# Kernel tuning notes

Measured on AMD Instinct MI355X. Metric: run time of the kernel, lower is better.

## Reference

```python
import jax, jax.numpy as jnp
import numpy as np

E = 32        # num_local_experts
TOP_K = 4     # num_experts_per_tok
H = 1024      # hidden_size
I = 1024      # intermediate_size (expert_dim)
ALPHA = 1.702
LIMIT = 7.0
B, S = 2, 1024


def setup_inputs() -> dict:
    key = jax.random.key(0)
    ks = jax.random.split(key, 8)
    scale = 0.02
    return {
        "hidden_states": jax.random.normal(ks[0], (B, S, H), dtype=jnp.float32),
        "gate_up_proj": jax.random.normal(ks[1], (E, H, 2 * I), dtype=jnp.float32) * scale,
        "gate_up_proj_bias": jax.random.normal(ks[2], (E, 2 * I), dtype=jnp.float32) * scale,
        "down_proj": jax.random.normal(ks[3], (E, I, H), dtype=jnp.float32) * scale,
        "down_proj_bias": jax.random.normal(ks[4], (E, H), dtype=jnp.float32) * scale,
        "router_weight": jax.random.normal(ks[5], (E, H), dtype=jnp.float32) * scale,
        "router_bias": jax.random.normal(ks[6], (E,), dtype=jnp.float32) * scale,
    }


def reference(hidden_states, gate_up_proj, gate_up_proj_bias, down_proj,
              down_proj_bias, router_weight, router_bias):
    b, s, h = hidden_states.shape
    x = hidden_states.reshape(-1, h)                       # [T, H], T = B*S
    t = x.shape[0]

    # ---- router: linear -> topk -> softmax over topk -> scatter to dense scores
    router_logits = x @ router_weight.T + router_bias      # [T, E]
    top_vals, top_idx = jax.lax.top_k(router_logits, TOP_K)
    top_w = jax.nn.softmax(top_vals, axis=-1)
    router_scores = jnp.zeros_like(router_logits).at[
        jnp.arange(t)[:, None], top_idx].set(top_w)        # [T, E]

    # ---- experts (dense all-expert path, interleaved gate/up columns)
    gate_w = gate_up_proj[..., 0::2]                       # [E, H, I]
    up_w = gate_up_proj[..., 1::2]                         # [E, H, I]
    gate_b = gate_up_proj_bias[..., 0::2]                  # [E, I]
    up_b = gate_up_proj_bias[..., 1::2]                    # [E, I]

    gate = jnp.einsum('th,ehi->eti', x, gate_w) + gate_b[:, None, :]
    up = jnp.einsum('th,ehi->eti', x, up_w) + up_b[:, None, :]
    gate = jnp.minimum(gate, LIMIT)
    up = jnp.clip(up, -LIMIT, LIMIT)
    glu = gate * jax.nn.sigmoid(gate * ALPHA)
    next_states = jnp.einsum('eti,eih->eth', (up + 1.0) * glu, down_proj)
    next_states = next_states + down_proj_bias[:, None, :]  # [E, T, H]

    # ---- combine: weight each expert output by its routing score and sum
    routed = jnp.einsum('eth,te->th', next_states, router_scores)
    return routed.reshape(b, s, h), router_scores
```

## Files before the change

kernel.cpp:

```cpp
#include <hip/hip_runtime.h>
#include <cstdint>
#include <cstddef>

#define E_ 32
#define TOPK_ 4
#define H_ 1024
#define I_ 1024
#define T_ 2048
#define ALPHA_ 1.702f
#define LIMIT_ 7.0f
#define BK_ 32
#define BKP_ 40

typedef __attribute__((ext_vector_type(8))) short s8;
typedef __attribute__((ext_vector_type(4))) float f4;

__device__ __forceinline__ unsigned short f2bf(float f) {
  unsigned int u = __float_as_uint(f);
  return (unsigned short)((u + 0x7fffu + ((u >> 16) & 1u)) >> 16);
}

__global__ __launch_bounds__(128)
void router_kernel(const float* __restrict__ x,
                   const float* __restrict__ rw,
                   const float* __restrict__ rb,
                   float* __restrict__ scores,
                   int* __restrict__ counts,
                   int* __restrict__ tok_list,
                   float* __restrict__ w_list) {
  int t = blockIdx.x;
  int tid = threadIdx.x;
  __shared__ float partial[128];
  __shared__ float logits[E_];
  int e = tid & 31, q = tid >> 5;
  const float* xp = x + (size_t)t * H_;
  const float* wp = rw + (size_t)e * H_ + q * 256;
  float s = 0.f;
  #pragma unroll 8
  for (int h = 0; h < 256; ++h) s += xp[q * 256 + h] * wp[h];
  partial[tid] = s;
  __syncthreads();
  if (tid < 32)
    logits[tid] = partial[tid] + partial[tid + 32] + partial[tid + 64] +
                  partial[tid + 96] + rb[tid];
  __syncthreads();
  if (tid == 0) {
    float l[E_];
    #pragma unroll
    for (int i = 0; i < E_; ++i) l[i] = logits[i];
    int idx[TOPK_]; float v[TOPK_];
    for (int k = 0; k < TOPK_; ++k) {
      int bi = 0; float bv = -1e30f;
      for (int i = 0; i < E_; ++i)
        if (l[i] > bv) { bv = l[i]; bi = i; }
      idx[k] = bi; v[k] = bv; l[bi] = -1e30f;
    }
    float m = v[0], den = 0.f, w[TOPK_];
    for (int k = 0; k < TOPK_; ++k) { w[k] = expf(v[k] - m); den += w[k]; }
    float inv = 1.f / den;
    float* srow = scores + (size_t)t * E_;
    #pragma unroll
    for (int i = 0; i < E_; ++i) srow[i] = 0.f;
    for (int k = 0; k < TOPK_; ++k) {
      float wk = w[k] * inv;
      srow[idx[k]] = wk;
      int pos = atomicAdd(&counts[idx[k]], 1);
      tok_list[idx[k] * T_ + pos] = t * TOPK_ + k;
      w_list[idx[k] * T_ + pos] = wk;
    }
  }
}

__global__ __launch_bounds__(256)
void gateup_mfma(const float* __restrict__ x,
                 const float* __restrict__ gw,
                 const float* __restrict__ gb,
                 const int* __restrict__ counts,
                 const int* __restrict__ tok_list,
                 unsigned short* __restrict__ act) {
  int e = blockIdx.z;
  int cnt = counts[e];
  int t0 = blockIdx.y * 64;
  if (t0 >= cnt) return;
  int itile = blockIdx.x;
  int tid = threadIdx.x;
  int lane = tid & 63;
  int wave = tid >> 6;
  int wm = wave >> 1, wn = wave & 1;

  __shared__ __align__(16) unsigned short Xs[2][64][BKP_];
  __shared__ __align__(16) unsigned short Wg[2][128][BKP_];
  __shared__ int toks[64];

  if (tid < 64) {
    int slot = t0 + tid;
    toks[tid] = (slot < cnt) ? tok_list[e * T_ + slot] : -1;
  }
  __syncthreads();

  f4 accg[2][2] = {};
  f4 accu[2][2] = {};

  int arow = tid >> 2;
  int akq  = (tid & 3) * 8;
  int aenc = toks[arow];
  const float* axp = (aenc >= 0) ? (x + (size_t)(aenc >> 2) * H_ + akq) : nullptr;
  const float* wbase = gw + (size_t)e * H_ * (2 * I_) + itile * 128;
  int n0 = tid & 127, koct0 = tid >> 7;
  int drow0 = (n0 >> 1) + (n0 & 1) * 64;
  const float* wp0 = wbase + (size_t)koct0 * 8 * (2 * I_) + n0;

  int fm = lane & 15, ko = (lane >> 4) * 8;

  float pA[8];
  float pB[2][8];

  {
    if (aenc >= 0) {
      float4 q0 = *(const float4*)(axp);
      float4 q1 = *(const float4*)(axp + 4);
      pA[0]=q0.x; pA[1]=q0.y; pA[2]=q0.z; pA[3]=q0.w;
      pA[4]=q1.x; pA[5]=q1.y; pA[6]=q1.z; pA[7]=q1.w;
    }
    #pragma unroll
    for (int r = 0; r < 2; ++r) {
      const float* wp = wp0 + (size_t)r * 16 * (2 * I_);
      #pragma unroll
      for (int j = 0; j < 8; ++j) pB[r][j] = wp[(size_t)j * (2 * I_)];
    }
  }

  int buf = 0;
  for (int c = 0; c < H_ / BK_; ++c) {
    {
      s8 av = {};
      if (aenc >= 0) {
        #pragma unroll
        for (int j = 0; j < 8; ++j) av[j] = (short)f2bf(pA[j]);
      }
      *(s8*)&Xs[buf][arow][akq] = av;
      #pragma unroll
      for (int r = 0; r < 2; ++r) {
        s8 bv;
        #pragma unroll
        for (int j = 0; j < 8; ++j) bv[j] = (short)f2bf(pB[r][j]);
        *(s8*)&Wg[buf][drow0][(koct0 + r * 2) * 8] = bv;
      }
    }
    __syncthreads();
    if (c + 1 < H_ / BK_) {
      int k0 = (c + 1) * BK_;
      if (aenc >= 0) {
        float4 q0 = *(const float4*)(axp + k0);
        float4 q1 = *(const float4*)(axp + k0 + 4);
        pA[0]=q0.x; pA[1]=q0.y; pA[2]=q0.z; pA[3]=q0.w;
        pA[4]=q1.x; pA[5]=q1.y; pA[6]=q1.z; pA[7]=q1.w;
      }
      #pragma unroll
      for (int r = 0; r < 2; ++r) {
        const float* wp = wp0 + (size_t)(k0 + r * 16) * (2 * I_);
        #pragma unroll
        for (int j = 0; j < 8; ++j) pB[r][j] = wp[(size_t)j * (2 * I_)];
      }
    }
    {
      s8 a0 = *(s8*)&Xs[buf][wm * 32 + fm][ko];
      s8 a1 = *(s8*)&Xs[buf][wm * 32 + 16 + fm][ko];
      #pragma unroll
      for (int g = 0; g < 2; ++g) {
        s8 bg = *(s8*)&Wg[buf][wn * 32 + g * 16 + fm][ko];
        s8 bu = *(s8*)&Wg[buf][64 + wn * 32 + g * 16 + fm][ko];
        accg[0][g] = __builtin_amdgcn_mfma_f32_16x16x32_bf16(a0, bg, accg[0][g], 0, 0, 0);
        accg[1][g] = __builtin_amdgcn_mfma_f32_16x16x32_bf16(a1, bg, accg[1][g], 0, 0, 0);
        accu[0][g] = __builtin_amdgcn_mfma_f32_16x16x32_bf16(a0, bu, accu[0][g], 0, 0, 0);
        accu[1][g] = __builtin_amdgcn_mfma_f32_16x16x32_bf16(a1, bu, accu[1][g], 0, 0, 0);
      }
    }
    buf ^= 1;
  }

  int rq = lane >> 4;
  #pragma unroll
  for (int g = 0; g < 2; ++g) {
    int i = itile * 64 + wn * 32 + g * 16 + (lane & 15);
    float bg_ = gb[e * 2 * I_ + 2 * i];
    float bu_ = gb[e * 2 * I_ + 2 * i + 1];
    #pragma unroll
    for (int f = 0; f < 2; ++f) {
      #pragma unroll
      for (int r = 0; r < 4; ++r) {
        int m = wm * 32 + f * 16 + rq * 4 + r;
        int enc = toks[m];
        if (enc < 0) continue;
        float gv = accg[f][g][r] + bg_;
        float uv = accu[f][g][r] + bu_;
        gv = fminf(gv, LIMIT_);
        uv = fminf(fmaxf(uv, -LIMIT_), LIMIT_);
        float glu = gv / (1.f + __expf(-ALPHA_ * gv));
        act[(size_t)enc * I_ + i] = f2bf((uv + 1.f) * glu);
      }
    }
  }
}

__global__ __launch_bounds__(256)
void down_mfma(const unsigned short* __restrict__ act,
               const float* __restrict__ dw,
               const float* __restrict__ db,
               const int* __restrict__ counts,
               const int* __restrict__ tok_list,
               const float* __restrict__ w_list,
               float* __restrict__ dsout) {
  int e = blockIdx.z;
  int cnt = counts[e];
  int t0 = blockIdx.y * 64;
  if (t0 >= cnt) return;
  int htile = blockIdx.x;
  int tid = threadIdx.x;
  int lane = tid & 63;
  int wave = tid >> 6;
  int wm = wave >> 1, wn = wave & 1;

  __shared__ __align__(16) unsigned short Xs[2][64][BKP_];
  __shared__ __align__(16) unsigned short Wd[2][128][BKP_];
  __shared__ int toks[64];
  __shared__ float tws[64];

  if (tid < 64) {
    int slot = t0 + tid;
    bool ok = slot < cnt;
    toks[tid] = ok ? tok_list[e * T_ + slot] : -1;
    tws[tid]  = ok ? w_list[e * T_ + slot] : 0.f;
  }
  __syncthreads();

  f4 acc[2][4] = {};

  int arow = tid >> 2;
  int akq  = (tid & 3) * 8;
  int aenc = toks[arow];
  const unsigned short* axp = (aenc >= 0) ? (act + (size_t)aenc * I_ + akq) : nullptr;
  const float* wbase = dw + (size_t)e * I_ * H_ + htile * 128;
  int n0 = tid & 127, koct0 = tid >> 7;
  const float* wp0 = wbase + (size_t)koct0 * 8 * H_ + n0;

  int fm = lane & 15, ko = (lane >> 4) * 8;

  s8 pA = {};
  float pB[2][8];

  {
    if (aenc >= 0) pA = *(const s8*)(axp);
    #pragma unroll
    for (int r = 0; r < 2; ++r) {
      const float* wp = wp0 + (size_t)r * 16 * H_;
      #pragma unroll
      for (int j = 0; j < 8; ++j) pB[r][j] = wp[(size_t)j * H_];
    }
  }

  int buf = 0;
  for (int c = 0; c < I_ / BK_; ++c) {
    *(s8*)&Xs[buf][arow][akq] = pA;
    #pragma unroll
    for (int r = 0; r < 2; ++r) {
      s8 bv;
      #pragma unroll
      for (int j = 0; j < 8; ++j) bv[j] = (short)f2bf(pB[r][j]);
      *(s8*)&Wd[buf][n0][(koct0 + r * 2) * 8] = bv;
    }
    __syncthreads();
    if (c + 1 < I_ / BK_) {
      int k0 = (c + 1) * BK_;
      if (aenc >= 0) pA = *(const s8*)(axp + k0);
      #pragma unroll
      for (int r = 0; r < 2; ++r) {
        const float* wp = wp0 + (size_t)(k0 + r * 16) * H_;
        #pragma unroll
        for (int j = 0; j < 8; ++j) pB[r][j] = wp[(size_t)j * H_];
      }
    }
    {
      s8 a0 = *(s8*)&Xs[buf][wm * 32 + fm][ko];
      s8 a1 = *(s8*)&Xs[buf][wm * 32 + 16 + fm][ko];
      #pragma unroll
      for (int g = 0; g < 4; ++g) {
        s8 b = *(s8*)&Wd[buf][wn * 64 + g * 16 + fm][ko];
        acc[0][g] = __builtin_amdgcn_mfma_f32_16x16x32_bf16(a0, b, acc[0][g], 0, 0, 0);
        acc[1][g] = __builtin_amdgcn_mfma_f32_16x16x32_bf16(a1, b, acc[1][g], 0, 0, 0);
      }
    }
    buf ^= 1;
  }

  int rq = lane >> 4;
  #pragma unroll
  for (int g = 0; g < 4; ++g) {
    int h = htile * 128 + wn * 64 + g * 16 + (lane & 15);
    float bias = db[e * H_ + h];
    #pragma unroll
    for (int f = 0; f < 2; ++f) {
      #pragma unroll
      for (int r = 0; r < 4; ++r) {
        int m = wm * 32 + f * 16 + rq * 4 + r;
        int enc = toks[m];
        if (enc < 0) continue;
        dsout[(size_t)enc * H_ + h] = (acc[f][g][r] + bias) * tws[m];
      }
    }
  }
}

__global__ __launch_bounds__(256)
void combine_kernel(const float* __restrict__ dsout,
                    float* __restrict__ routed) {
  int idx = blockIdx.x * 256 + threadIdx.x;
  int t = idx >> 8;
  int h = (idx & 255) * 4;
  const float* base = dsout + (size_t)t * 4 * H_ + h;
  float4 a = *(const float4*)(base);
  float4 b = *(const float4*)(base + H_);
  float4 c = *(const float4*)(base + 2 * H_);
  float4 d = *(const float4*)(base + 3 * H_);
  float4 o;
  o.x = a.x + b.x + c.x + d.x;
  o.y = a.y + b.y + c.y + d.y;
  o.z = a.z + b.z + c.z + d.z;
  o.w = a.w + b.w + c.w + d.w;
  *(float4*)(routed + (size_t)t * H_ + h) = o;
}

extern "C" void kernel_launch(void* const* d_in, const int* in_sizes, int n_in,
                              void* d_out, int out_size, void* d_ws, size_t ws_size,
                              hipStream_t stream) {
  (void)in_sizes; (void)n_in; (void)out_size; (void)ws_size;
  const float* x    = (const float*)d_in[0];
  const float* gup  = (const float*)d_in[1];
  const float* gupb = (const float*)d_in[2];
  const float* dwn  = (const float*)d_in[3];
  const float* dwnb = (const float*)d_in[4];
  const float* rw   = (const float*)d_in[5];
  const float* rb   = (const float*)d_in[6];

  float* routed = (float*)d_out;
  float* scores = (float*)d_out + (size_t)T_ * H_;

  char* ws = (char*)d_ws;
  int*   counts   = (int*)ws;
  int*   tok_list = (int*)(ws + 256);
  float* w_list   = (float*)(ws + 256 + (size_t)E_ * T_ * 4);
  unsigned short* act = (unsigned short*)(ws + 256 + 2 * (size_t)E_ * T_ * 4);
  float* dsout = (float*)(ws + 256 + 2 * (size_t)E_ * T_ * 4
                          + (size_t)T_ * TOPK_ * I_ * 2);

  hipMemsetAsync(counts, 0, E_ * sizeof(int), stream);

  router_kernel<<<T_, 128, 0, stream>>>(x, rw, rb, scores, counts, tok_list, w_list);
  gateup_mfma<<<dim3(16, 32, 32), 256, 0, stream>>>(x, gup, gupb, counts, tok_list, act);
  down_mfma<<<dim3(8, 32, 32), 256, 0, stream>>>(act, dwn, dwnb, counts, tok_list, w_list, dsout);
  combine_kernel<<<(T_ * H_ / 4) / 256, 256, 0, stream>>>(dsout, routed);
}
```

Baseline: 674.3 us.

## Pre-transpose and cast expert weights to bf16 before the MFMA GEMMs

Adds pre-pass kernels that cast activations to bf16 and transpose/cast the gate-up weights (de-interleaving gate and up) and the down weights into K-contiguous bf16 layouts. The GEMM kernels can then load 16-byte bf16 vectors directly into LDS instead of doing strided scalar fp32 loads and per-block conversion repeated across token tiles. The router dot product is also vectorized with float4 loads. The trade-off is an extra full read of the fp32 weights and a bf16 write every call, and the down-GEMM output buffer now reuses the gate-up weight scratch region.

```diff
diff --git a/kernel.cpp b/kernel.cpp
--- a/kernel.cpp
+++ b/kernel.cpp
@@ -11,6 +11,7 @@
 #define LIMIT_ 7.0f
 #define BK_ 32
 #define BKP_ 40
+#define TP_ 66
 
 typedef __attribute__((ext_vector_type(8))) short s8;
 typedef __attribute__((ext_vector_type(4))) float f4;
@@ -18,6 +19,60 @@
 __device__ __forceinline__ unsigned short f2bf(float f) {
   unsigned int u = __float_as_uint(f);
   return (unsigned short)((u + 0x7fffu + ((u >> 16) & 1u)) >> 16);
+}
+
+__global__ __launch_bounds__(256)
+void cast_x_kernel(const float* __restrict__ x, unsigned short* __restrict__ xb) {
+  size_t i = (size_t)(blockIdx.x * 256 + threadIdx.x) * 8;
+  float4 a = *(const float4*)(x + i);
+  float4 b = *(const float4*)(x + i + 4);
+  s8 v;
+  v[0] = (short)f2bf(a.x); v[1] = (short)f2bf(a.y);
+  v[2] = (short)f2bf(a.z); v[3] = (short)f2bf(a.w);
+  v[4] = (short)f2bf(b.x); v[5] = (short)f2bf(b.y);
+  v[6] = (short)f2bf(b.z); v[7] = (short)f2bf(b.w);
+  *(s8*)(xb + i) = v;
+}
+
+__global__ __launch_bounds__(256)
+void transpose_cast(const float* __restrict__ src, unsigned short* __restrict__ dst,
+                    int src_rows, int src_cols, int deint) {
+  int e = blockIdx.z;
+  int c0 = blockIdx.x * 64;
+  int r0 = blockIdx.y * 64;
+  int tid = threadIdx.x;
+  __shared__ unsigned short ldsT[64][TP_];
+
+  const float* sp = src + (size_t)e * src_rows * src_cols
+                        + (size_t)r0 * src_cols + c0;
+  int r = tid >> 2, cq = tid & 3;
+  const float* rowp = sp + (size_t)r * src_cols + cq * 4;
+  #pragma unroll
+  for (int j = 0; j < 4; ++j) {
+    float4 v = *(const float4*)(rowp + j * 16);
+    int c = cq * 4 + j * 16;
+    ldsT[c + 0][r] = f2bf(v.x);
+    ldsT[c + 1][r] = f2bf(v.y);
+    ldsT[c + 2][r] = f2bf(v.z);
+    ldsT[c + 3][r] = f2bf(v.w);
+  }
+  __syncthreads();
+
+  int co = tid >> 2, hq = tid & 3;
+  s8 v0 = *(s8*)&ldsT[co][hq * 16];
+  s8 v1 = *(s8*)&ldsT[co][hq * 16 + 8];
+  int C = c0 + co;
+  size_t out_off;
+  if (deint) {
+    out_off = (size_t)e * src_cols * src_rows
+            + (size_t)(C & 1) * (src_cols >> 1) * src_rows
+            + (size_t)(C >> 1) * src_rows + r0 + hq * 16;
+  } else {
+    out_off = (size_t)e * src_cols * src_rows
+            + (size_t)C * src_rows + r0 + hq * 16;
+  }
+  *(s8*)(dst + out_off) = v0;
+  *(s8*)(dst + out_off + 8) = v1;
 }
 
 __global__ __launch_bounds__(128)
@@ -33,11 +88,14 @@
   __shared__ float partial[128];
   __shared__ float logits[E_];
   int e = tid & 31, q = tid >> 5;
-  const float* xp = x + (size_t)t * H_;
-  const float* wp = rw + (size_t)e * H_ + q * 256;
+  const float4* xp = (const float4*)(x + (size_t)t * H_ + q * 256);
+  const float4* wp = (const float4*)(rw + (size_t)e * H_ + q * 256);
   float s = 0.f;
   #pragma unroll 8
-  for (int h = 0; h < 256; ++h) s += xp[q * 256 + h] * wp[h];
+  for (int h = 0; h < 64; ++h) {
+    float4 a = xp[h], b = wp[h];
+    s += a.x * b.x + a.y * b.y + a.z * b.z + a.w * b.w;
+  }
   partial[tid] = s;
   __syncthreads();
   if (tid < 32)
@@ -72,8 +130,8 @@
 }
 
 __global__ __launch_bounds__(256)
-void gateup_mfma(const float* __restrict__ x,
-                 const float* __restrict__ gw,
+void gateup_mfma(const unsigned short* __restrict__ xb,
+                 const unsigned short* __restrict__ wgu,
                  const float* __restrict__ gb,
                  const int* __restrict__ counts,
                  const int* __restrict__ tok_list,
@@ -101,67 +159,32 @@
   f4 accg[2][2] = {};
   f4 accu[2][2] = {};
 
-  int arow = tid >> 2;
-  int akq  = (tid & 3) * 8;
-  int aenc = toks[arow];
-  const float* axp = (aenc >= 0) ? (x + (size_t)(aenc >> 2) * H_ + akq) : nullptr;
-  const float* wbase = gw + (size_t)e * H_ * (2 * I_) + itile * 128;
-  int n0 = tid & 127, koct0 = tid >> 7;
-  int drow0 = (n0 >> 1) + (n0 & 1) * 64;
-  const float* wp0 = wbase + (size_t)koct0 * 8 * (2 * I_) + n0;
+  int row = tid >> 2, q = tid & 3;
+  int aenc = toks[row];
+  const unsigned short* axp = xb + (size_t)(aenc >> 2) * H_ + q * 8;
+  const unsigned short* bp0 = wgu + (size_t)e * 2 * I_ * H_
+                            + (size_t)(itile * 64 + row) * H_ + q * 8;
+  const unsigned short* bp1 = bp0 + (size_t)I_ * H_;
 
   int fm = lane & 15, ko = (lane >> 4) * 8;
 
-  float pA[8];
-  float pB[2][8];
-
-  {
-    if (aenc >= 0) {
-      float4 q0 = *(const float4*)(axp);
-      float4 q1 = *(const float4*)(axp + 4);
-      pA[0]=q0.x; pA[1]=q0.y; pA[2]=q0.z; pA[3]=q0.w;
-      pA[4]=q1.x; pA[5]=q1.y; pA[6]=q1.z; pA[7]=q1.w;
-    }
-    #pragma unroll
-    for (int r = 0; r < 2; ++r) {
-      const float* wp = wp0 + (size_t)r * 16 * (2 * I_);
-      #pragma unroll
-      for (int j = 0; j < 8; ++j) pB[r][j] = wp[(size_t)j * (2 * I_)];
-    }
-  }
+  s8 pA = {};
+  s8 pB0, pB1;
+  if (aenc >= 0) pA = *(const s8*)axp;
+  pB0 = *(const s8*)bp0;
+  pB1 = *(const s8*)bp1;
 
   int buf = 0;
   for (int c = 0; c < H_ / BK_; ++c) {
-    {
-      s8 av = {};
-      if (aenc >= 0) {
-        #pragma unroll
-        for (int j = 0; j < 8; ++j) av[j] = (short)f2bf(pA[j]);
-      }
-      *(s8*)&Xs[buf][arow][akq] = av;
-      #pragma unroll
-      for (int r = 0; r < 2; ++r) {
-        s8 bv;
-        #pragma unroll
-        for (int j = 0; j < 8; ++j) bv[j] = (short)f2bf(pB[r][j]);
-        *(s8*)&Wg[buf][drow0][(koct0 + r * 2) * 8] = bv;
-      }
-    }
+    *(s8*)&Xs[buf][row][q * 8] = pA;
+    *(s8*)&Wg[buf][row][q * 8] = pB0;
+    *(s8*)&Wg[buf][64 + row][q * 8] = pB1;
     __syncthreads();
     if (c + 1 < H_ / BK_) {
       int k0 = (c + 1) * BK_;
-      if (aenc >= 0) {
-        float4 q0 = *(const float4*)(axp + k0);
-        float4 q1 = *(const float4*)(axp + k0 + 4);
-        pA[0]=q0.x; pA[1]=q0.y; pA[2]=q0.z; pA[3]=q0.w;
-        pA[4]=q1.x; pA[5]=q1.y; pA[6]=q1.z; pA[7]=q1.w;
-      }
-      #pragma unroll
-      for (int r = 0; r < 2; ++r) {
-        const float* wp = wp0 + (size_t)(k0 + r * 16) * (2 * I_);
-        #pragma unroll
-        for (int j = 0; j < 8; ++j) pB[r][j] = wp[(size_t)j * (2 * I_)];
-      }
+      if (aenc >= 0) pA = *(const s8*)(axp + k0);
+      pB0 = *(const s8*)(bp0 + k0);
+      pB1 = *(const s8*)(bp1 + k0);
     }
     {
       s8 a0 = *(s8*)&Xs[buf][wm * 32 + fm][ko];
@@ -205,7 +228,7 @@
 
 __global__ __launch_bounds__(256)
 void down_mfma(const unsigned short* __restrict__ act,
-               const float* __restrict__ dw,
+               const unsigned short* __restrict__ wdt,
                const float* __restrict__ db,
                const int* __restrict__ counts,
                const int* __restrict__ tok_list,
@@ -236,49 +259,32 @@
 
   f4 acc[2][4] = {};
 
-  int arow = tid >> 2;
-  int akq  = (tid & 3) * 8;
-  int aenc = toks[arow];
-  const unsigned short* axp = (aenc >= 0) ? (act + (size_t)aenc * I_ + akq) : nullptr;
-  const float* wbase = dw + (size_t)e * I_ * H_ + htile * 128;
-  int n0 = tid & 127, koct0 = tid >> 7;
-  const float* wp0 = wbase + (size_t)koct0 * 8 * H_ + n0;
+  int row = tid >> 2, q = tid & 3;
+  int aenc = toks[row];
+  const unsigned short* axp = act + (size_t)aenc * I_ + q * 8;
+  const unsigned short* bp0 = wdt + (size_t)e * H_ * I_
+                            + (size_t)(htile * 128 + row) * I_ + q * 8;
+  const unsigned short* bp1 = bp0 + (size_t)64 * I_;
 
   int fm = lane & 15, ko = (lane >> 4) * 8;
 
   s8 pA = {};
-  float pB[2][8];
-
-  {
-    if (aenc >= 0) pA = *(const s8*)(axp);
-    #pragma unroll
-    for (int r = 0; r < 2; ++r) {
-      const float* wp = wp0 + (size_t)r * 16 * H_;
-      #pragma unroll
-      for (int j = 0; j < 8; ++j) pB[r][j] = wp[(size_t)j * H_];
-    }
-  }
+  s8 pB0, pB1;
+  if (aenc >= 0) pA = *(const s8*)axp;
+  pB0 = *(const s8*)bp0;
+  pB1 = *(const s8*)bp1;
 
   int buf = 0;
   for (int c = 0; c < I_ / BK_; ++c) {
-    *(s8*)&Xs[buf][arow][akq] = pA;
-    #pragma unroll
-    for (int r = 0; r < 2; ++r) {
-      s8 bv;
-      #pragma unroll
-      for (int j = 0; j < 8; ++j) bv[j] = (short)f2bf(pB[r][j]);
-      *(s8*)&Wd[buf][n0][(koct0 + r * 2) * 8] = bv;
-    }
+    *(s8*)&Xs[buf][row][q * 8] = pA;
+    *(s8*)&Wd[buf][row][q * 8] = pB0;
+    *(s8*)&Wd[buf][64 + row][q * 8] = pB1;
     __syncthreads();
     if (c + 1 < I_ / BK_) {
       int k0 = (c + 1) * BK_;
       if (aenc >= 0) pA = *(const s8*)(axp + k0);
-      #pragma unroll
-      for (int r = 0; r < 2; ++r) {
-        const float* wp = wp0 + (size_t)(k0 + r * 16) * H_;
-        #pragma unroll
-        for (int j = 0; j < 8; ++j) pB[r][j] = wp[(size_t)j * H_];
-      }
+      pB0 = *(const s8*)(bp0 + k0);
+      pB1 = *(const s8*)(bp1 + k0);
     }
     {
       s8 a0 = *(s8*)&Xs[buf][wm * 32 + fm][ko];
@@ -347,16 +353,26 @@
 
   char* ws = (char*)d_ws;
   int*   counts   = (int*)ws;
-  int*   tok_list = (int*)(ws + 256);
-  float* w_list   = (float*)(ws + 256 + (size_t)E_ * T_ * 4);
-  unsigned short* act = (unsigned short*)(ws + 256 + 2 * (size_t)E_ * T_ * 4);
-  float* dsout = (float*)(ws + 256 + 2 * (size_t)E_ * T_ * 4
-                          + (size_t)T_ * TOPK_ * I_ * 2);
+  int*   tok_list = (int*)(ws + ((size_t)1 << 20));
+  float* w_list   = (float*)(ws + ((size_t)1 << 20) + (size_t)E_ * T_ * 4);
+  unsigned short* xbf = (unsigned short*)(ws + ((size_t)2 << 20));
+  unsigned short* act = (unsigned short*)(ws + ((size_t)8 << 20));
+  unsigned short* wgu_b = (unsigned short*)(ws + ((size_t)24 << 20));
+  float*          dsout = (float*)(ws + ((size_t)24 << 20));
+  unsigned short* wdt_b = (unsigned short*)(ws + ((size_t)24 << 20)
+                                            + (size_t)E_ * 2 * I_ * H_ * 2);
 
   hipMemsetAsync(counts, 0, E_ * sizeof(int), stream);
 
+  cast_x_kernel<<<(T_ * H_ / 8) / 256, 256, 0, stream>>>(x, xbf);
+  transpose_cast<<<dim3(2 * I_ / 64, H_ / 64, E_), 256, 0, stream>>>(
+      gup, wgu_b, H_, 2 * I_, 1);
+  transpose_cast<<<dim3(H_ / 64, I_ / 64, E_), 256, 0, stream>>>(
+      dwn, wdt_b, I_, H_, 0);
   router_kernel<<<T_, 128, 0, stream>>>(x, rw, rb, scores, counts, tok_list, w_list);
-  gateup_mfma<<<dim3(16, 32, 32), 256, 0, stream>>>(x, gup, gupb, counts, tok_list, act);
-  down_mfma<<<dim3(8, 32, 32), 256, 0, stream>>>(act, dwn, dwnb, counts, tok_list, w_list, dsout);
+  gateup_mfma<<<dim3(16, 32, 32), 256, 0, stream>>>(xbf, wgu_b, gupb,
+                                                    counts, tok_list, act);
+  down_mfma<<<dim3(8, 32, 32), 256, 0, stream>>>(act, wdt_b, dwnb,
+                                                 counts, tok_list, w_list, dsout);
   combine_kernel<<<(T_ * H_ / 4) / 256, 256, 0, stream>>>(dsout, routed);
 }
```

Result: slower. 729.2 us (+8.1%).
